# Kernel optimization log

Measured on AMD Instinct MI355X. Metric: run time of the kernel, lower is better.

The kernel has to match this reference:

```python
import jax, jax.numpy as jnp
import numpy as np

B, T, C = 8, 2048, 1024
HEAD = 64
BLOCK = 2048  # block_size == max_size == ramp_size


def setup_inputs() -> dict:
    key = jax.random.key(0)
    kx, kq, kk, kv = jax.random.split(key, 4)
    x = jax.random.normal(kx, (B, T, C), dtype=jnp.float32)
    # torch Linear(n_embd, head_size, bias=False): store as (C, HEAD) for x @ W
    s = 1.0 / np.sqrt(C)
    Wq = jax.random.uniform(kq, (C, HEAD), dtype=jnp.float32, minval=-s, maxval=s)
    Wk = jax.random.uniform(kk, (C, HEAD), dtype=jnp.float32, minval=-s, maxval=s)
    Wv = jax.random.uniform(kv, (C, HEAD), dtype=jnp.float32, minval=-s, maxval=s)
    # adaptive_span current_val parameter, shape (1,1,1), init 0
    current_val = jnp.zeros((1, 1, 1), dtype=jnp.float32)
    return {"x": x, "Wq": Wq, "Wk": Wk, "Wv": Wv, "current_val": current_val}


def reference(x, Wq, Wk, Wv, current_val):
    Bb, Tt, Cc = x.shape
    q = x @ Wq  # (B,T,H)
    k = x @ Wk
    v = x @ Wv
    scale = 1.0 / jnp.sqrt(jnp.asarray(HEAD, dtype=x.dtype))
    scores = jnp.einsum('bth,bsh->bts', q, k) * scale  # (B,T,T)
    causal = jnp.tril(jnp.ones((Tt, Tt), dtype=bool))
    scores = jnp.where(causal, scores, -jnp.inf)
    w = jax.nn.softmax(scores, axis=-1)
    # adaptive span post-softmax mask (T == max_size here, so no slicing)
    template = jnp.linspace(1.0 - BLOCK, 0.0, BLOCK, dtype=x.dtype)  # (T,)
    span = template + current_val * BLOCK  # (1,1,T)
    span = jnp.clip(span / BLOCK + 1.0, 0.0, 1.0)
    w = w * span
    w = w / (w.sum(-1, keepdims=True) + 1e-8)
    # dropout p=0 (eval) -> identity
    out = jnp.einsum('bts,bsh->bth', w, v)  # (B,T,H)
    return out
```

## Files before the change

kernel.cpp:

```cpp
#include <hip/hip_runtime.h>
#include <hip/hip_bf16.h>

#define BSZ 8
#define T 2048
#define C 1024
#define H 64
#define M (BSZ*T)

typedef __attribute__((ext_vector_type(4))) float f32x4;
typedef __attribute__((ext_vector_type(8))) short bf16x8;
typedef __attribute__((ext_vector_type(4))) short s16x4;
typedef __attribute__((ext_vector_type(8))) short s16x8;

static __device__ __forceinline__ short f2bf(float f) {
  union { float f; unsigned u; } c; c.f = f;
  unsigned u = c.u;
  u = (u + 0x7fffu + ((u >> 16) & 1u)) >> 16;
  return (short)u;
}

__global__ __launch_bounds__(256) void k_wt(const float* __restrict__ Wq,
                                            const float* __restrict__ Wk,
                                            const float* __restrict__ Wv,
                                            short* __restrict__ wt) {
  int idx = blockIdx.x * 256 + threadIdx.x;
  int c = idx & (C - 1);
  int n = idx >> 10;
  int w = n >> 6;
  int h = n & (H - 1);
  const float* W = (w == 0) ? Wq : (w == 1) ? Wk : Wv;
  wt[idx] = f2bf(W[c * H + h]);
}

__global__ __launch_bounds__(256) void k_qkv(const float* __restrict__ x,
                                             const short* __restrict__ wt,
                                             short* __restrict__ qb,
                                             short* __restrict__ kb,
                                             short* __restrict__ vt) {
  __shared__ short xs[2][32 * 64];
  __shared__ short wl[2][192 * 64];
  const int tid = threadIdx.x;
  const int m0 = blockIdx.x * 32;
  const int lane = tid & 63;
  const int wid = tid >> 6;
  const int g16 = lane >> 4, l16 = lane & 15;
  const int row0 = (wid & 1) * 16;
  const int nc0 = (wid >> 1) * 96;

  f32x4 acc[6];
  #pragma unroll
  for (int i = 0; i < 6; ++i) acc[i] = (f32x4){0.f, 0.f, 0.f, 0.f};

  const int xr = tid >> 4;
  const int xc4 = (tid & 15) * 4;
  const int xsw = xc4 ^ ((xr & 7) << 3);
  const int wr = tid >> 3;
  const int wc8 = (tid & 7) * 8;
  const int wsw = wc8 ^ ((wr & 7) << 3);
  const int fsw = (l16 & 7) << 3;

  float4 xA0, xA1, xB0, xB1;
  s16x8 wA0, wA1, wA2, wA3, wA4, wA5;
  s16x8 wB0, wB1, wB2, wB3, wB4, wB5;

#define QKV_LOAD(S, kc) do { \
    x##S##0 = *(const float4*)&x[(size_t)(m0 + xr) * C + (kc) + xc4]; \
    x##S##1 = *(const float4*)&x[(size_t)(m0 + xr + 16) * C + (kc) + xc4]; \
    w##S##0 = *(const s16x8*)&wt[(wr +   0) * C + (kc) + wc8]; \
    w##S##1 = *(const s16x8*)&wt[(wr +  32) * C + (kc) + wc8]; \
    w##S##2 = *(const s16x8*)&wt[(wr +  64) * C + (kc) + wc8]; \
    w##S##3 = *(const s16x8*)&wt[(wr +  96) * C + (kc) + wc8]; \
    w##S##4 = *(const s16x8*)&wt[(wr + 128) * C + (kc) + wc8]; \
    w##S##5 = *(const s16x8*)&wt[(wr + 160) * C + (kc) + wc8]; \
  } while (0)

#define QKV_STORE(S, buf) do { \
    s16x4 h0 = { f2bf((x##S##0).x), f2bf((x##S##0).y), f2bf((x##S##0).z), f2bf((x##S##0).w) }; \
    s16x4 h1 = { f2bf((x##S##1).x), f2bf((x##S##1).y), f2bf((x##S##1).z), f2bf((x##S##1).w) }; \
    *(s16x4*)&xs[buf][xr * 64 + xsw] = h0; \
    *(s16x4*)&xs[buf][(xr + 16) * 64 + xsw] = h1; \
    *(s16x8*)&wl[buf][(wr +   0) * 64 + wsw] = w##S##0; \
    *(s16x8*)&wl[buf][(wr +  32) * 64 + wsw] = w##S##1; \
    *(s16x8*)&wl[buf][(wr +  64) * 64 + wsw] = w##S##2; \
    *(s16x8*)&wl[buf][(wr +  96) * 64 + wsw] = w##S##3; \
    *(s16x8*)&wl[buf][(wr + 128) * 64 + wsw] = w##S##4; \
    *(s16x8*)&wl[buf][(wr + 160) * 64 + wsw] = w##S##5; \
  } while (0)

#define QKV_COMPUTE(buf) do { \
    _Pragma("unroll") \
    for (int ks = 0; ks < 2; ++ks) { \
      bf16x8 a = *(const bf16x8*)&xs[buf][(row0 + l16) * 64 + ((ks * 32 + g16 * 8) ^ fsw)]; \
      _Pragma("unroll") \
      for (int nt = 0; nt < 6; ++nt) { \
        bf16x8 bfr = *(const bf16x8*)&wl[buf][(nc0 + nt * 16 + l16) * 64 + ((ks * 32 + g16 * 8) ^ fsw)]; \
        acc[nt] = __builtin_amdgcn_mfma_f32_16x16x32_bf16(a, bfr, acc[nt], 0, 0, 0); \
      } \
    } \
  } while (0)

  QKV_LOAD(A, 0);
  QKV_STORE(A, 0);
  QKV_LOAD(B, 64);
  __syncthreads();

  #pragma unroll 1
  for (int ii = 0; ii < 8; ++ii) {
    if (ii < 7) QKV_LOAD(A, (2 * ii + 2) * 64);
    QKV_STORE(B, 1);
    QKV_COMPUTE(0);
    __syncthreads();
    if (ii < 7) {
      QKV_LOAD(B, (2 * ii + 3) * 64);
      QKV_STORE(A, 0);
    }
    QKV_COMPUTE(1);
    if (ii < 7) __syncthreads();
  }
#undef QKV_LOAD
#undef QKV_STORE
#undef QKV_COMPUTE

  const int r0 = row0 + g16 * 4;
  #pragma unroll
  for (int nt = 0; nt < 6; ++nt) {
    const int nglob = nc0 + nt * 16;
    const int which = nglob >> 6;
    const int col = (nglob & 63) + l16;
    #pragma unroll
    for (int j = 0; j < 4; ++j) {
      const int tg = m0 + r0 + j;
      const short val = f2bf(acc[nt][j]);
      if (which == 0)      qb[tg * H + col] = val;
      else if (which == 1) kb[tg * H + col] = val;
      else {
        const int b = tg >> 11, tl = tg & (T - 1);
        vt[((b << 6) + col) * T + tl] = val;
      }
    }
  }
}

__global__ __launch_bounds__(512, 4) void k_attn(const short* __restrict__ qb,
                                                 const short* __restrict__ kb,
                                                 const short* __restrict__ vt,
                                                 const float* __restrict__ cvp,
                                                 float* __restrict__ out) {
  __shared__ __align__(16) char smem[34816];
  short (*plds)[2][16][40] = (short (*)[2][16][40])smem;
  float (*Ow)[16][68]      = (float (*)[16][68])smem;
  __shared__ float mw[8][16];
  __shared__ float Lw[8][16];
  const int blk = blockIdx.x;
  const int b = blk & 7;
  const int t = 127 - (blk >> 3);
  const int q0 = t << 4;
  const int tid = threadIdx.x;
  const int wid = tid >> 6;
  const int lane = tid & 63;
  const int g16 = lane >> 4, l16 = lane & 15;
  const float cv = cvp[0];
  const float SCL = 0.125f * 1.44269504f;

  const int nit = (q0 + 16 + 31) >> 5;
  const int npw = (nit + 7) >> 3;
  const int lo = wid * npw;
  const int hi = (lo + npw < nit) ? lo + npw : nit;

  const short* qp = qb + ((size_t)(b << 11) + q0 + l16) * H + g16 * 8;
  bf16x8 qf0 = *(const bf16x8*)qp;
  bf16x8 qf1 = *(const bf16x8*)(qp + 32);
  const int qg = q0 + l16;

  float m = -3e38f, L = 0.f;
  f32x4 O[4];
  #pragma unroll
  for (int t4 = 0; t4 < 4; ++t4) O[t4] = (f32x4){0.f, 0.f, 0.f, 0.f};

  if (lo < hi) {
    const short* kp = kb + ((size_t)(b << 11) + lo * 32 + l16) * H + g16 * 8;
    const short* vp = vt + ((size_t)(b << 6) + l16) * T + lo * 32 + g16 * 8;
    bf16x8 kc0 = *(const bf16x8*)kp;
    bf16x8 kc1 = *(const bf16x8*)(kp + 32);
    bf16x8 kc2 = *(const bf16x8*)(kp + 16 * H);
    bf16x8 kc3 = *(const bf16x8*)(kp + 16 * H + 32);
    kp += 32 * H;

    for (int it = lo; it < hi; ++it) {
      bf16x8 kn0, kn1, kn2, kn3;
      const bool more = (it + 1 < hi);
      if (more) {
        kn0 = *(const bf16x8*)kp;
        kn1 = *(const bf16x8*)(kp + 32);
        kn2 = *(const bf16x8*)(kp + 16 * H);
        kn3 = *(const bf16x8*)(kp + 16 * H + 32);
      }
      bf16x8 v0 = *(const bf16x8*)vp;
      bf16x8 v1 = *(const bf16x8*)(vp + 16 * T);
      bf16x8 v2 = *(const bf16x8*)(vp + 32 * T);
      bf16x8 v3 = *(const bf16x8*)(vp + 48 * T);

      f32x4 s0 = {0.f,0.f,0.f,0.f}, s1 = {0.f,0.f,0.f,0.f};
      s0 = __builtin_amdgcn_mfma_f32_16x16x32_bf16(kc0, qf0, s0, 0, 0, 0);
      s0 = __builtin_amdgcn_mfma_f32_16x16x32_bf16(kc1, qf1, s0, 0, 0, 0);
      s1 = __builtin_amdgcn_mfma_f32_16x16x32_bf16(kc2, qf0, s1, 0, 0, 0);
      s1 = __builtin_amdgcn_mfma_f32_16x16x32_bf16(kc3, qf1, s1, 0, 0, 0);

      const int kv0 = it << 5;
      const int kvb = kv0 + g16 * 4;
      const bool diag = (kv0 + 31 > q0);
      float sv[8];
      if (diag) {
        #pragma unroll
        for (int r = 0; r < 8; ++r) {
          const int kvg = kvb + ((r >> 2) << 4) + (r & 3);
          const float s = ((r < 4) ? s0[r] : s1[r - 4]) * SCL;
          sv[r] = (kvg <= qg) ? s : -1e30f;
        }
      } else {
        #pragma unroll
        for (int r = 0; r < 8; ++r)
          sv[r] = ((r < 4) ? s0[r] : s1[r - 4]) * SCL;
      }

      float pmax = fmaxf(fmaxf(fmaxf(sv[0], sv[1]), fmaxf(sv[2], sv[3])),
                         fmaxf(fmaxf(sv[4], sv[5]), fmaxf(sv[6], sv[7])));
      if (!__all(pmax <= m + 7.f)) {
        float v = pmax;
        v = fmaxf(v, __shfl_xor(v, 16, 64));
        v = fmaxf(v, __shfl_xor(v, 32, 64));
        const float mn = fmaxf(m, v);
        const float al = exp2f(m - mn);
        m = mn;
        L *= al;
        #pragma unroll
        for (int t4 = 0; t4 < 4; ++t4) O[t4] *= al;
      }

      float p[8];
      #pragma unroll
      for (int r = 0; r < 8; ++r) {
        const int kvg = kvb + ((r >> 2) << 4) + (r & 3);
        const float sp = fminf(fmaxf((float)(kvg + 1) * (1.f / 2048.f) + cv, 0.f), 1.f);
        p[r] = exp2f(sv[r] - m) * sp;
      }
      if (diag) {
        #pragma unroll
        for (int r = 0; r < 8; ++r) {
          const int kvg = kvb + ((r >> 2) << 4) + (r & 3);
          p[r] = (kvg <= qg) ? p[r] : 0.f;
        }
      }
      L += ((p[0] + p[1]) + (p[2] + p[3])) + ((p[4] + p[5]) + (p[6] + p[7]));

      short (*pl)[40] = plds[wid][it & 1];
      #pragma unroll
      for (int r = 0; r < 8; r += 2) {
        union { float f; unsigned u; } a0, a1;
        a0.f = p[r]; a1.f = p[r + 1];
        const unsigned pk = (a0.u >> 16) | (a1.u & 0xffff0000u);
        *(unsigned*)&pl[l16][((r >> 2) << 4) + g16 * 4 + (r & 3)] = pk;
      }
      bf16x8 pa = *(const bf16x8*)&pl[l16][g16 * 8];
      O[0] = __builtin_amdgcn_mfma_f32_16x16x32_bf16(v0, pa, O[0], 0, 0, 0);
      O[1] = __builtin_amdgcn_mfma_f32_16x16x32_bf16(v1, pa, O[1], 0, 0, 0);
      O[2] = __builtin_amdgcn_mfma_f32_16x16x32_bf16(v2, pa, O[2], 0, 0, 0);
      O[3] = __builtin_amdgcn_mfma_f32_16x16x32_bf16(v3, pa, O[3], 0, 0, 0);

      if (more) { kc0 = kn0; kc1 = kn1; kc2 = kn2; kc3 = kn3; }
      kp += 32 * H;
      vp += 32;
    }
  }

  __syncthreads();

  float Lr = L;
  Lr += __shfl_xor(Lr, 16, 64);
  Lr += __shfl_xor(Lr, 32, 64);
  if (g16 == 0) { mw[wid][l16] = m; Lw[wid][l16] = Lr; }
  #pragma unroll
  for (int t4 = 0; t4 < 4; ++t4)
    *(f32x4*)&Ow[wid][l16][t4 * 16 + g16 * 4] = O[t4];
  __syncthreads();

  if (tid < 256) {
    const int r = tid >> 4;
    const int c4 = (tid & 15) << 2;
    float Mx = -3e38f;
    #pragma unroll
    for (int w = 0; w < 8; ++w) Mx = fmaxf(Mx, mw[w][r]);
    float f[8], Ls = 0.f;
    #pragma unroll
    for (int w = 0; w < 8; ++w) {
      f[w] = exp2f(mw[w][r] - Mx);
      Ls += Lw[w][r] * f[w];
    }
    f32x4 o = (f32x4){0.f, 0.f, 0.f, 0.f};
    #pragma unroll
    for (int w = 0; w < 8; ++w) {
      f32x4 ow = *(const f32x4*)&Ow[w][r][c4];
      o += ow * f[w];
    }
    o *= 1.f / (Ls + 1e-30f);
    *(f32x4*)&out[(size_t)((b << 11) + q0 + r) * H + c4] = o;
  }
}

extern "C" void kernel_launch(void* const* d_in, const int* in_sizes, int n_in,
                              void* d_out, int out_size, void* d_ws, size_t ws_size,
                              hipStream_t stream) {
  const float* x  = (const float*)d_in[0];
  const float* Wq = (const float*)d_in[1];
  const float* Wk = (const float*)d_in[2];
  const float* Wv = (const float*)d_in[3];
  const float* cv = (const float*)d_in[4];
  float* out = (float*)d_out;

  char* ws = (char*)d_ws;
  short* qb = (short*)(ws);
  short* kb = (short*)(ws + (size_t)M * H * 2);
  short* vt = (short*)(ws + (size_t)2 * M * H * 2);
  short* wt = (short*)(ws + (size_t)3 * M * H * 2);

  hipLaunchKernelGGL(k_wt, dim3(3 * H * C / 256), dim3(256), 0, stream, Wq, Wk, Wv, wt);
  hipLaunchKernelGGL(k_qkv, dim3(M / 32), dim3(256), 0, stream, x, wt, qb, kb, vt);
  hipLaunchKernelGGL(k_attn, dim3(BSZ * T / 16), dim3(512), 0, stream, qb, kb, vt, cv, out);
}
```

Baseline: 66.03 us.

## Pair short and long causal query tiles per block to balance attention work

Each attention block now handles two 16-row query tiles, one from the start and one from the end of the causal range. The 8 waves are split between the two tiles in proportion to their key-iteration counts. The final merge now uses all 512 threads to combine partial results for 32 rows. The grid is halved. The aim is to even out per-block work under the causal mask and reduce the tail imbalance across blocks. The cost is fewer blocks in flight, uneven integer wave splits, and runtime-bounded merge loops that are no longer unrolled.

```diff
diff --git a/kernel.cpp b/kernel.cpp
--- a/kernel.cpp
+++ b/kernel.cpp
@@ -151,10 +151,17 @@
   float (*Ow)[16][68]      = (float (*)[16][68])smem;
   __shared__ float mw[8][16];
   __shared__ float Lw[8][16];
-  const int blk = blockIdx.x;
-  const int b = blk & 7;
-  const int t = 127 - (blk >> 3);
-  const int q0 = t << 4;
+  const int pid = blockIdx.x;
+  const int b = pid & 7;
+  const int pr = pid >> 3;
+  const int tA = pr, tB = 127 - pr;
+  const int q0A = tA << 4, q0B = tB << 4;
+  const int nitA = (q0A + 47) >> 5;
+  const int nitB = (q0B + 47) >> 5;
+  const int NT = nitA + nitB;
+  int wA = (8 * nitA + (NT >> 1)) / NT;
+  wA = wA < 1 ? 1 : (wA > 7 ? 7 : wA);
+
   const int tid = threadIdx.x;
   const int wid = tid >> 6;
   const int lane = tid & 63;
@@ -162,10 +169,14 @@
   const float cv = cvp[0];
   const float SCL = 0.125f * 1.44269504f;
 
-  const int nit = (q0 + 16 + 31) >> 5;
-  const int npw = (nit + 7) >> 3;
-  const int lo = wid * npw;
-  const int hi = (lo + npw < nit) ? lo + npw : nit;
+  const bool onA = (wid < wA);
+  const int q0 = onA ? q0A : q0B;
+  const int nitW = onA ? nitA : nitB;
+  const int nwt = onA ? wA : 8 - wA;
+  const int wg = onA ? wid : wid - wA;
+  const int npw = (nitW + nwt - 1) / nwt;
+  const int lo = wg * npw;
+  const int hi = (lo + npw < nitW) ? lo + npw : nitW;
 
   const short* qp = qb + ((size_t)(b << 11) + q0 + l16) * H + g16 * 8;
   bf16x8 qf0 = *(const bf16x8*)qp;
@@ -284,26 +295,26 @@
     *(f32x4*)&Ow[wid][l16][t4 * 16 + g16 * 4] = O[t4];
   __syncthreads();
 
-  if (tid < 256) {
-    const int r = tid >> 4;
+  {
+    const int r32 = tid >> 4;
     const int c4 = (tid & 15) << 2;
+    const bool rowA = (r32 < 16);
+    const int r = rowA ? r32 : r32 - 16;
+    const int w0 = rowA ? 0 : wA;
+    const int w1 = rowA ? wA : 8;
+    const int q0r = rowA ? q0A : q0B;
     float Mx = -3e38f;
-    #pragma unroll
-    for (int w = 0; w < 8; ++w) Mx = fmaxf(Mx, mw[w][r]);
-    float f[8], Ls = 0.f;
-    #pragma unroll
-    for (int w = 0; w < 8; ++w) {
-      f[w] = exp2f(mw[w][r] - Mx);
-      Ls += Lw[w][r] * f[w];
-    }
+    for (int w = w0; w < w1; ++w) Mx = fmaxf(Mx, mw[w][r]);
+    float Ls = 0.f;
     f32x4 o = (f32x4){0.f, 0.f, 0.f, 0.f};
-    #pragma unroll
-    for (int w = 0; w < 8; ++w) {
+    for (int w = w0; w < w1; ++w) {
+      const float fw = exp2f(mw[w][r] - Mx);
+      Ls += Lw[w][r] * fw;
       f32x4 ow = *(const f32x4*)&Ow[w][r][c4];
-      o += ow * f[w];
+      o += ow * fw;
     }
     o *= 1.f / (Ls + 1e-30f);
-    *(f32x4*)&out[(size_t)((b << 11) + q0 + r) * H + c4] = o;
+    *(f32x4*)&out[(size_t)((b << 11) + q0r + r) * H + c4] = o;
   }
 }
 
@@ -325,5 +336,5 @@
 
   hipLaunchKernelGGL(k_wt, dim3(3 * H * C / 256), dim3(256), 0, stream, Wq, Wk, Wv, wt);
   hipLaunchKernelGGL(k_qkv, dim3(M / 32), dim3(256), 0, stream, x, wt, qb, kb, vt);
-  hipLaunchKernelGGL(k_attn, dim3(BSZ * T / 16), dim3(512), 0, stream, qb, kb, vt, cv, out);
-}
+  hipLaunchKernelGGL(k_attn, dim3(BSZ * T / 32), dim3(512), 0, stream, qb, kb, vt, cv, out);
+}
```

Result: faster. 63.40 us (median of 4 runs) (-4.0%).
